# Optimization experiments

Hardware: AMD Instinct MI355X
Metric: run time of the kernel (lower is better)

Reference implementation:

```python
import jax, jax.numpy as jnp
import numpy as np

N_NODES = 100000
N_EDGES = 1600000
NUM_FEATURES = 128
NHID = 64
HIDDEN = 2 * NHID  # GATConv out_channels = nhid*2 = 128
NUM_CLASSES = 2
NUM_GRAPHS = 64
NEG_SLOPE = 0.2  # PyG GATConv default


def setup_inputs() -> dict:
    key = jax.random.key(0)
    ks = jax.random.split(key, 16)
    x = jax.random.normal(ks[0], (N_NODES, NUM_FEATURES), dtype=jnp.float32)
    edge_index = jax.random.randint(ks[1], (2, N_EDGES), 0, N_NODES, dtype=jnp.int64)
    batch = jnp.sort(jax.random.randint(ks[2], (N_NODES,), 0, NUM_GRAPHS, dtype=jnp.int64))
    def glorot(k, shape):
        lim = np.sqrt(6.0 / (shape[0] + shape[1]))
        return jax.random.uniform(k, shape, jnp.float32, -lim, lim)
    W1 = glorot(ks[3], (NUM_FEATURES, HIDDEN))
    a_src1 = glorot(ks[4], (HIDDEN, 1))[:, 0]
    a_dst1 = glorot(ks[5], (HIDDEN, 1))[:, 0]
    b1 = jnp.zeros((HIDDEN,), jnp.float32)
    W2 = glorot(ks[6], (HIDDEN, HIDDEN))
    a_src2 = glorot(ks[7], (HIDDEN, 1))[:, 0]
    a_dst2 = glorot(ks[8], (HIDDEN, 1))[:, 0]
    b2 = jnp.zeros((HIDDEN,), jnp.float32)
    fc1_w = glorot(ks[9], (HIDDEN, NHID))
    fc1_b = jnp.zeros((NHID,), jnp.float32)
    fc2_w = glorot(ks[10], (NHID, NUM_CLASSES))
    fc2_b = jnp.zeros((NUM_CLASSES,), jnp.float32)
    return {"x": x, "edge_index": edge_index, "batch": batch,
            "W1": W1, "a_src1": a_src1, "a_dst1": a_dst1, "b1": b1,
            "W2": W2, "a_src2": a_src2, "a_dst2": a_dst2, "b2": b2,
            "fc1_w": fc1_w, "fc1_b": fc1_b, "fc2_w": fc2_w, "fc2_b": fc2_b}


def gat_conv(x, src, dst, W, a_src, a_dst, b, n_nodes):
    # PyG GATConv, heads=1, add_self_loops=True: message flows src -> dst
    h = x @ W                                   # [N, H]
    alpha_s = h @ a_src                         # [N]
    alpha_d = h @ a_dst                         # [N]
    e = jax.nn.leaky_relu(alpha_s[src] + alpha_d[dst], NEG_SLOPE)  # [E2]
    m = jax.ops.segment_max(e, dst, num_segments=n_nodes)          # per-dst max
    ex = jnp.exp(e - m[dst])
    z = jax.ops.segment_sum(ex, dst, num_segments=n_nodes)
    alpha = ex / z[dst]                         # segment softmax over incoming edges
    out = jax.ops.segment_sum(h[src] * alpha[:, None], dst, num_segments=n_nodes)
    return out + b


def reference(x, edge_index, batch, W1, a_src1, a_dst1, b1,
              W2, a_src2, a_dst2, b2, fc1_w, fc1_b, fc2_w, fc2_b):
    n = x.shape[0]
    loop = jnp.arange(n, dtype=edge_index.dtype)
    src = jnp.concatenate([edge_index[0], loop])  # add self-loops (PyG default)
    dst = jnp.concatenate([edge_index[1], loop])
    h = jax.nn.selu(gat_conv(x, src, dst, W1, a_src1, a_dst1, b1, n))
    h = jax.nn.selu(gat_conv(h, src, dst, W2, a_src2, a_dst2, b2, n))
    # global mean pool over graphs
    sums = jax.ops.segment_sum(h, batch, num_segments=NUM_GRAPHS)
    cnt = jax.ops.segment_sum(jnp.ones((n,), h.dtype), batch, num_segments=NUM_GRAPHS)
    pooled = jax.nn.selu(sums / jnp.maximum(cnt, 1.0)[:, None])
    feat = jax.nn.selu(pooled @ fc1_w + fc1_b)   # dropout is identity in eval
    logits = feat @ fc2_w + fc2_b
    return logits, feat
```

## Files before the change

kernel.cpp:

```cpp
#include <hip/hip_runtime.h>
#include <hip/hip_bf16.h>

#define N_NODES 100000
#define N_EDGES 1600000
#define E_TOT   (N_EDGES + N_NODES)
#define F 128
#define NGRAPH 64
#define NEG_SLOPE 0.2f
#define SELU_SCALE 1.0507009873554805f
#define SELU_ALPHA 1.6732632423543772f

#define BSZ 256
#define NB  391
#define CAP 5120
#define CHUNK 4096
#define NCHUNK 416
#define LCAP 5120
#define PCHUNK 32

typedef __attribute__((ext_vector_type(8))) short bf16x8;
typedef __attribute__((ext_vector_type(4))) float f32x4;

__device__ __forceinline__ float selu_f(float x) {
    return x > 0.f ? SELU_SCALE * x : SELU_SCALE * SELU_ALPHA * (__expf(x) - 1.f);
}
__device__ __forceinline__ float lrelu(float x) {
    return x > 0.f ? x : NEG_SLOPE * x;
}
__device__ __forceinline__ unsigned short f2bf(float f) {
    unsigned u = __float_as_uint(f);
    return (unsigned short)((u + 0x7FFFu + ((u >> 16) & 1u)) >> 16);
}
__device__ __forceinline__ float bfval(unsigned short u) {
    return __uint_as_float(((unsigned)u) << 16);
}
__device__ __forceinline__ float ub0(unsigned w) { return (float)(w & 0xffu); }
__device__ __forceinline__ float ub1(unsigned w) { return (float)((w >> 8) & 0xffu); }
__device__ __forceinline__ float ub2(unsigned w) { return (float)((w >> 16) & 0xffu); }
__device__ __forceinline__ float ub3(unsigned w) { return (float)(w >> 24); }

__global__ __launch_bounds__(256) void init_k(int* __restrict__ cursor,
                                              float* __restrict__ gsum) {
    int i = blockIdx.x * 256 + threadIdx.x;
    if (i < NB) cursor[i] = i * CAP;
    if (i < NGRAPH * F) gsum[i] = 0.f;
}

__global__ __launch_bounds__(256) void pack_w2(const float* __restrict__ W1,
                                               const float* __restrict__ W2,
                                               unsigned short* __restrict__ W1f,
                                               unsigned short* __restrict__ W2f) {
    int i = blockIdx.x * 256 + threadIdx.x;
    const float* W = (i < 2048) ? W1 : W2;
    unsigned short* Wf = (i < 2048) ? W1f : W2f;
    int ii = i & 2047;
    int l = ii & 63, t = (ii >> 6) & 3, nt = ii >> 8;
    int kb = t * 32 + (l >> 4) * 8;
    int n  = nt * 16 + (l & 15);
    unsigned short o[8];
#pragma unroll
    for (int j = 0; j < 8; ++j) o[j] = f2bf(W[(size_t)(kb + j) * F + n]);
    uint4 p;
    p.x = ((unsigned)o[1] << 16) | o[0];
    p.y = ((unsigned)o[3] << 16) | o[2];
    p.z = ((unsigned)o[5] << 16) | o[4];
    p.w = ((unsigned)o[7] << 16) | o[6];
    ((uint4*)Wf)[ii] = p;
}

template <bool XF32>
__global__ __launch_bounds__(256) void gemm_mfma(const void* __restrict__ Xin,
                                                 const unsigned short* __restrict__ Wf,
                                                 const float* __restrict__ avs,
                                                 const float* __restrict__ avd,
                                                 unsigned char* __restrict__ Hq,
                                                 float2* __restrict__ asc,
                                                 float* __restrict__ ad_) {
    int w = threadIdx.x >> 6, l = threadIdx.x & 63;
    int row0 = blockIdx.x * 64 + w * 16;
    int arow = row0 + (l & 15);
    int arow_c = arow < N_NODES ? arow : N_NODES - 1;
    f32x4 acc[8] = {};
#pragma unroll
    for (int t = 0; t < 4; ++t) {
        bf16x8 a;
        if (XF32) {
            const float* Xf = (const float*)Xin + (size_t)arow_c * F + t * 32 + (l >> 4) * 8;
            float4 v0 = *(const float4*)Xf;
            float4 v1 = *(const float4*)(Xf + 4);
            a[0] = (short)f2bf(v0.x); a[1] = (short)f2bf(v0.y);
            a[2] = (short)f2bf(v0.z); a[3] = (short)f2bf(v0.w);
            a[4] = (short)f2bf(v1.x); a[5] = (short)f2bf(v1.y);
            a[6] = (short)f2bf(v1.z); a[7] = (short)f2bf(v1.w);
        } else {
            a = *(const bf16x8*)((const unsigned short*)Xin +
                                 (size_t)arow_c * F + t * 32 + (l >> 4) * 8);
        }
#pragma unroll
        for (int nt = 0; nt < 8; ++nt) {
            bf16x8 b = *(const bf16x8*)(Wf + (size_t)((nt * 4 + t) * 64 + l) * 8);
            acc[nt] = __builtin_amdgcn_mfma_f32_16x16x32_bf16(a, b, acc[nt], 0, 0, 0);
        }
    }
    int c = l & 15;
    float ps[4] = {}, pd[4] = {}, mx[4] = {};
#pragma unroll
    for (int nt = 0; nt < 8; ++nt) {
        float ws = avs[nt * 16 + c];
        float wd = avd[nt * 16 + c];
#pragma unroll
        for (int r = 0; r < 4; ++r) {
            ps[r] += acc[nt][r] * ws;
            pd[r] += acc[nt][r] * wd;
            mx[r] = fmaxf(mx[r], fabsf(acc[nt][r]));
        }
    }
#pragma unroll
    for (int r = 0; r < 4; ++r) {
#pragma unroll
        for (int off = 1; off < 16; off <<= 1) {
            ps[r] += __shfl_xor(ps[r], off);
            pd[r] += __shfl_xor(pd[r], off);
            mx[r] = fmaxf(mx[r], __shfl_xor(mx[r], off));
        }
    }
#pragma unroll
    for (int r = 0; r < 4; ++r) {
        int grow = row0 + (l >> 4) * 4 + r;
        if (grow >= N_NODES) continue;
        float inv = mx[r] > 0.f ? 127.f / mx[r] : 0.f;
#pragma unroll
        for (int nt = 0; nt < 8; ++nt) {
            int q = (int)rintf(acc[nt][r] * inv) + 128;
            Hq[(size_t)grow * F + nt * 16 + c] = (unsigned char)q;
        }
        if (c == 0) {
            asc[grow] = make_float2(ps[r], mx[r] * (1.f / 127.f));
            ad_[grow] = pd[r];
        }
    }
}

__global__ __launch_bounds__(256) void scatter1(const int* __restrict__ ei,
                                                int* __restrict__ cursor,
                                                unsigned* __restrict__ packed) {
    __shared__ int lh[NB], lbase[NB];
    for (int i = threadIdx.x; i < NB; i += 256) lh[i] = 0;
    __syncthreads();
    int base = blockIdx.x * CHUNK;
#pragma unroll
    for (int k = 0; k < 16; ++k) {
        int i = base + k * 256 + threadIdx.x;
        if (i < E_TOT) {
            int d = (i < N_EDGES) ? ei[N_EDGES + i] : i - N_EDGES;
            atomicAdd(&lh[d >> 8], 1);
        }
    }
    __syncthreads();
    for (int i = threadIdx.x; i < NB; i += 256) {
        int cn = lh[i];
        lbase[i] = cn ? atomicAdd(&cursor[i], cn) : 0;
        lh[i] = 0;
    }
    __syncthreads();
#pragma unroll
    for (int k = 0; k < 16; ++k) {
        int i = base + k * 256 + threadIdx.x;
        if (i < E_TOT) {
            int s, d;
            if (i < N_EDGES) { s = ei[i]; d = ei[N_EDGES + i]; }
            else             { s = d = i - N_EDGES; }
            int b = d >> 8;
            int r = atomicAdd(&lh[b], 1);
            int pos = lbase[b] + r;
            if (pos < (b + 1) * CAP)
                packed[pos] = (unsigned)s | ((unsigned)(d & 255) << 20);
        }
    }
}

__global__ __launch_bounds__(256) void build2(const int* __restrict__ cursor,
                                              const unsigned* __restrict__ packed,
                                              int2* __restrict__ rsd,
                                              int* __restrict__ csr_src) {
    __shared__ int sh_hist[BSZ], sh_row[BSZ], ts[BSZ];
    __shared__ int lsrc[LCAP];
    int b = blockIdx.x, t = threadIdx.x;
    int node0 = b << 8;
    int nn = min(BSZ, N_NODES - node0);
    int base = b * CAP;
    int cnt = min(cursor[b] - base, CAP);
    sh_hist[t] = 0;
    __syncthreads();
    for (int j = t; j < cnt; j += 256)
        atomicAdd(&sh_hist[packed[base + j] >> 20], 1);
    __syncthreads();
    int dv = sh_hist[t];
    ts[t] = dv;
    __syncthreads();
    for (int off = 1; off < 256; off <<= 1) {
        int u = (t >= off) ? ts[t - off] : 0;
        __syncthreads();
        ts[t] += u;
        __syncthreads();
    }
    sh_row[t] = ts[t] - dv;
    if (t < nn) rsd[node0 + t] = make_int2(base + sh_row[t], dv);
    sh_hist[t] = 0;
    __syncthreads();
    for (int j = t; j < cnt; j += 256) {
        unsigned u = packed[base + j];
        int dlo = u >> 20;
        int r = atomicAdd(&sh_hist[dlo], 1);
        lsrc[sh_row[dlo] + r] = (int)(u & 0xFFFFFu);
    }
    __syncthreads();
    for (int j = t; j < cnt; j += 256) csr_src[base + j] = lsrc[j];
}

__global__ __launch_bounds__(256) void gat2(const int2* __restrict__ rsd,
                                            const int* __restrict__ csr_src,
                                            const float2* __restrict__ asc,
                                            const float* __restrict__ ad_,
                                            const unsigned char* __restrict__ Hq,
                                            const float* __restrict__ bias,
                                            unsigned short* __restrict__ outb) {
    int wid = (blockIdx.x * 256 + threadIdx.x) >> 6;
    int lane = threadIdx.x & 63;
    int vbase = wid * 2;
    if (vbase >= N_NODES) return;
    const int hb = lane & 32;
    const int j  = lane & 31;
    const unsigned* HqI = (const unsigned*)Hq;
    int vown = vbase + (lane >> 5);

    int2 rv = rsd[vown];
    int start = rv.x, deg = rv.y;
    int dmax = max(deg, __shfl_xor(deg, 32));

    if (dmax <= 32) {
        int s_reg = 0;
        float2 a2 = make_float2(0.f, 0.f);
        float ev = -__builtin_inff();
        if (j < deg) {
            s_reg = csr_src[start + j];
            a2 = asc[s_reg];
            ev = lrelu(a2.x + ad_[vown]);
        }
        float m = ev;
#pragma unroll
        for (int off = 1; off < 32; off <<= 1) m = fmaxf(m, __shfl_xor(m, off));
        float ex = (j < deg) ? __expf(ev - m) : 0.f;
        float zs = ex;
#pragma unroll
        for (int off = 1; off < 32; off <<= 1) zs += __shfl_xor(zs, off);
        float alsc = (ex / zs) * a2.y;

        float acc0 = 0.f, acc1 = 0.f, acc2 = 0.f, acc3 = 0.f, ksum = 0.f;
        int e = 0;
        for (; e + 8 <= dmax; e += 8) {
            float al[8]; int sv[8]; unsigned uw[8];
#pragma unroll
            for (int q = 0; q < 8; ++q) {
                al[q] = __shfl(alsc, hb | (e + q));
                sv[q] = __shfl(s_reg, hb | (e + q));
            }
#pragma unroll
            for (int q = 0; q < 8; ++q) uw[q] = HqI[(sv[q] << 5) + j];
#pragma unroll
            for (int q = 0; q < 8; ++q) {
                ksum += al[q];
                acc0 += ub0(uw[q]) * al[q];
                acc1 += ub1(uw[q]) * al[q];
                acc2 += ub2(uw[q]) * al[q];
                acc3 += ub3(uw[q]) * al[q];
            }
        }
        for (; e < dmax; ++e) {
            float al = __shfl(alsc, hb | e);
            int   s  = __shfl(s_reg, hb | e);
            unsigned uw = HqI[(s << 5) + j];
            ksum += al;
            acc0 += ub0(uw) * al; acc1 += ub1(uw) * al;
            acc2 += ub2(uw) * al; acc3 += ub3(uw) * al;
        }
        float4 bv = *(const float4*)(bias + j * 4);
        float r0 = selu_f(acc0 - 128.f * ksum + bv.x);
        float r1 = selu_f(acc1 - 128.f * ksum + bv.y);
        float r2 = selu_f(acc2 - 128.f * ksum + bv.z);
        float r3 = selu_f(acc3 - 128.f * ksum + bv.w);
        uint2 p;
        p.x = ((unsigned)f2bf(r1) << 16) | f2bf(r0);
        p.y = ((unsigned)f2bf(r3) << 16) | f2bf(r2);
        *(uint2*)(outb + (size_t)vown * F + j * 4) = p;
    } else {
        const int half = lane >> 5;
        const int fq = lane & 31;
        for (int sub = 0; sub < 2; ++sub) {
            int vv = vbase + sub;
            int2 r2v = rsd[vv];
            int st = r2v.x, dg = r2v.y;
            float adv = ad_[vv];
            float m = -__builtin_inff();
            for (int i = st + lane; i < st + dg; i += 64)
                m = fmaxf(m, lrelu(asc[csr_src[i]].x + adv));
#pragma unroll
            for (int off = 1; off < 64; off <<= 1) m = fmaxf(m, __shfl_xor(m, off));
            float zs = 0.f;
            for (int i = st + lane; i < st + dg; i += 64)
                zs += __expf(lrelu(asc[csr_src[i]].x + adv) - m);
#pragma unroll
            for (int off = 1; off < 64; off <<= 1) zs += __shfl_xor(zs, off);
            float zinv = 1.f / zs;
            float acc0 = 0.f, acc1 = 0.f, acc2 = 0.f, acc3 = 0.f, ksum = 0.f;
            int e = 0;
            for (; e + 2 <= dg; e += 2) {
                int s = csr_src[st + e + half];
                float2 a2 = asc[s];
                float al = __expf(lrelu(a2.x + adv) - m) * zinv * a2.y;
                unsigned uw = HqI[(s << 5) + fq];
                ksum += al;
                acc0 += ub0(uw) * al; acc1 += ub1(uw) * al;
                acc2 += ub2(uw) * al; acc3 += ub3(uw) * al;
            }
            if (e < dg && half == 0) {
                int s = csr_src[st + e];
                float2 a2 = asc[s];
                float al = __expf(lrelu(a2.x + adv) - m) * zinv * a2.y;
                unsigned uw = HqI[(s << 5) + fq];
                ksum += al;
                acc0 += ub0(uw) * al; acc1 += ub1(uw) * al;
                acc2 += ub2(uw) * al; acc3 += ub3(uw) * al;
            }
            acc0 += __shfl_xor(acc0, 32); acc1 += __shfl_xor(acc1, 32);
            acc2 += __shfl_xor(acc2, 32); acc3 += __shfl_xor(acc3, 32);
            ksum += __shfl_xor(ksum, 32);
            float4 bv = *(const float4*)(bias + fq * 4);
            float r0 = selu_f(acc0 - 128.f * ksum + bv.x);
            float r1 = selu_f(acc1 - 128.f * ksum + bv.y);
            float r2 = selu_f(acc2 - 128.f * ksum + bv.z);
            float r3 = selu_f(acc3 - 128.f * ksum + bv.w);
            if (half == 0) {
                uint2 p;
                p.x = ((unsigned)f2bf(r1) << 16) | f2bf(r0);
                p.y = ((unsigned)f2bf(r3) << 16) | f2bf(r2);
                *(uint2*)(outb + (size_t)vv * F + fq * 4) = p;
            }
        }
    }
}

__device__ __forceinline__ int lower_bound(const int* __restrict__ b, int v) {
    int lo = 0, hi = N_NODES;
    while (lo < hi) { int mid = (lo + hi) >> 1; if (b[mid] < v) lo = mid + 1; else hi = mid; }
    return lo;
}

__global__ __launch_bounds__(128) void pool_partial(const unsigned short* __restrict__ Xb,
                                                    const int* __restrict__ batch,
                                                    float* __restrict__ gsum) {
    int g = blockIdx.x / PCHUNK, c = blockIdx.x % PCHUNK;
    int start = lower_bound(batch, g);
    int end = lower_bound(batch, g + 1);
    int len = end - start;
    int s0 = start + (int)((long)len * c / PCHUNK);
    int s1 = start + (int)((long)len * (c + 1) / PCHUNK);
    if (s1 <= s0) return;
    int f = threadIdx.x;
    float sum = 0.f;
    for (int i = s0; i < s1; ++i)
        sum += bfval(Xb[(size_t)i * F + f]);
    atomicAdd(&gsum[g * F + f], sum);
}

__global__ __launch_bounds__(128) void pool_head(const float* __restrict__ gsum,
                                                 const int* __restrict__ batch,
                                                 const float* __restrict__ fc1w,
                                                 const float* __restrict__ fc1b,
                                                 const float* __restrict__ fc2w,
                                                 const float* __restrict__ fc2b,
                                                 float* __restrict__ out) {
    __shared__ float pooled[128];
    __shared__ float fs[64];
    __shared__ int bnd[2];
    int g = blockIdx.x, t = threadIdx.x;
    if (t < 2) bnd[t] = lower_bound(batch, g + t);
    __syncthreads();
    float c = fmaxf((float)(bnd[1] - bnd[0]), 1.f);
    pooled[t] = selu_f(gsum[g * F + t] / c);
    __syncthreads();
    if (t < 64) {
        float a = fc1b[t];
        for (int k = 0; k < F; ++k) a += pooled[k] * fc1w[k * 64 + t];
        float fv = selu_f(a);
        fs[t] = fv;
        out[128 + g * 64 + t] = fv;
    }
    __syncthreads();
    if (t < 2) {
        float l = fc2b[t];
        for (int k = 0; k < 64; ++k) l += fs[k] * fc2w[k * 2 + t];
        out[g * 2 + t] = l;
    }
}

extern "C" void kernel_launch(void* const* d_in, const int* in_sizes, int n_in,
                              void* d_out, int out_size, void* d_ws, size_t ws_size,
                              hipStream_t stream) {
    const float* x    = (const float*)d_in[0];
    const int*   ei   = (const int*)d_in[1];
    const int*   batch= (const int*)d_in[2];
    const float* W1   = (const float*)d_in[3];
    const float* as1  = (const float*)d_in[4];
    const float* ad1  = (const float*)d_in[5];
    const float* b1   = (const float*)d_in[6];
    const float* W2   = (const float*)d_in[7];
    const float* as2  = (const float*)d_in[8];
    const float* ad2  = (const float*)d_in[9];
    const float* b2   = (const float*)d_in[10];
    const float* fc1w = (const float*)d_in[11];
    const float* fc1b = (const float*)d_in[12];
    const float* fc2w = (const float*)d_in[13];
    const float* fc2b = (const float*)d_in[14];
    float* out = (float*)d_out;

    unsigned short* Xb   = (unsigned short*)d_ws;
    unsigned char*  Hq   = (unsigned char*)(Xb + (size_t)N_NODES * F);
    unsigned short* W1f  = (unsigned short*)(Hq + (size_t)N_NODES * F);
    unsigned short* W2f  = W1f + 16384;
    float2* asc   = (float2*)(W2f + 16384);
    float*  ad_   = (float*)(asc + N_NODES);
    int2*   rsd   = (int2*)(ad_ + N_NODES);
    int*    csr_src = (int*)(rsd + N_NODES);
    unsigned* packed = (unsigned*)(csr_src + NB * CAP);
    int*    cursor= (int*)(packed + NB * CAP);
    float*  gsum  = (float*)(cursor + NB + 64);

    const int gGemm = (N_NODES + 63) / 64;
    const int gGat  = (N_NODES + 7) / 8;

    init_k<<<32, 256, 0, stream>>>(cursor, gsum);
    pack_w2<<<16, 256, 0, stream>>>(W1, W2, W1f, W2f);

    scatter1<<<NCHUNK, 256, 0, stream>>>(ei, cursor, packed);
    build2<<<NB, 256, 0, stream>>>(cursor, packed, rsd, csr_src);

    gemm_mfma<true><<<gGemm, 256, 0, stream>>>(x, W1f, as1, ad1, Hq, asc, ad_);
    gat2<<<gGat, 256, 0, stream>>>(rsd, csr_src, asc, ad_, Hq, b1, Xb);

    gemm_mfma<false><<<gGemm, 256, 0, stream>>>(Xb, W2f, as2, ad2, Hq, asc, ad_);
    gat2<<<gGat, 256, 0, stream>>>(rsd, csr_src, asc, ad_, Hq, b2, Xb);

    pool_partial<<<NGRAPH * PCHUNK, 128, 0, stream>>>(Xb, batch, gsum);
    pool_head<<<NGRAPH, 128, 0, stream>>>(gsum, batch, fc1w, fc1b, fc2w, fc2b, out);
}
```

Baseline: 217.8 us.

## Split GAT aggregation into alpha pass and feature-slabbed gather over sliced Hq

The quantized feature matrix Hq is stored as 8 column slabs of 16 bytes per node instead of 128 contiguous bytes per node. The fused gat2 kernel is split in two. alpha2 computes the per-edge softmax weights and their per-node sum and writes them with the source index into an edge array. gat_slab then gathers one slab per block, so the random-access working set per block is about 1.6 MB of Hq rather than 12.8 MB and is meant to stay cache-resident. In exchange it adds a kernel launch, writes and reads an extra edge array of roughly 13.6 MB per layer, and rereads rsd and edata once per slab.

```diff
diff --git a/kernel.cpp b/kernel.cpp
--- a/kernel.cpp
+++ b/kernel.cpp
@@ -17,6 +17,7 @@
 #define NCHUNK 416
 #define LCAP 5120
 #define PCHUNK 32
+#define NSLAB 8
 
 typedef __attribute__((ext_vector_type(8))) short bf16x8;
 typedef __attribute__((ext_vector_type(4))) float f32x4;
@@ -132,7 +133,7 @@
 #pragma unroll
         for (int nt = 0; nt < 8; ++nt) {
             int q = (int)rintf(acc[nt][r] * inv) + 128;
-            Hq[(size_t)grow * F + nt * 16 + c] = (unsigned char)q;
+            Hq[(size_t)nt * N_NODES * 16 + (size_t)grow * 16 + c] = (unsigned char)q;
         }
         if (c == 0) {
             asc[grow] = make_float2(ps[r], mx[r] * (1.f / 127.f));
@@ -218,20 +219,17 @@
     for (int j = t; j < cnt; j += 256) csr_src[base + j] = lsrc[j];
 }
 
-__global__ __launch_bounds__(256) void gat2(const int2* __restrict__ rsd,
-                                            const int* __restrict__ csr_src,
-                                            const float2* __restrict__ asc,
-                                            const float* __restrict__ ad_,
-                                            const unsigned char* __restrict__ Hq,
-                                            const float* __restrict__ bias,
-                                            unsigned short* __restrict__ outb) {
+__global__ __launch_bounds__(256) void alpha2(const int2* __restrict__ rsd,
+                                              const int* __restrict__ csr_src,
+                                              const float2* __restrict__ asc,
+                                              const float* __restrict__ ad_,
+                                              uint2* __restrict__ edata,
+                                              float* __restrict__ ksum_) {
     int wid = (blockIdx.x * 256 + threadIdx.x) >> 6;
     int lane = threadIdx.x & 63;
     int vbase = wid * 2;
     if (vbase >= N_NODES) return;
-    const int hb = lane & 32;
-    const int j  = lane & 31;
-    const unsigned* HqI = (const unsigned*)Hq;
+    int j = lane & 31;
     int vown = vbase + (lane >> 5);
 
     int2 rv = rsd[vown];
@@ -255,47 +253,12 @@
 #pragma unroll
         for (int off = 1; off < 32; off <<= 1) zs += __shfl_xor(zs, off);
         float alsc = (ex / zs) * a2.y;
-
-        float acc0 = 0.f, acc1 = 0.f, acc2 = 0.f, acc3 = 0.f, ksum = 0.f;
-        int e = 0;
-        for (; e + 8 <= dmax; e += 8) {
-            float al[8]; int sv[8]; unsigned uw[8];
-#pragma unroll
-            for (int q = 0; q < 8; ++q) {
-                al[q] = __shfl(alsc, hb | (e + q));
-                sv[q] = __shfl(s_reg, hb | (e + q));
-            }
-#pragma unroll
-            for (int q = 0; q < 8; ++q) uw[q] = HqI[(sv[q] << 5) + j];
-#pragma unroll
-            for (int q = 0; q < 8; ++q) {
-                ksum += al[q];
-                acc0 += ub0(uw[q]) * al[q];
-                acc1 += ub1(uw[q]) * al[q];
-                acc2 += ub2(uw[q]) * al[q];
-                acc3 += ub3(uw[q]) * al[q];
-            }
-        }
-        for (; e < dmax; ++e) {
-            float al = __shfl(alsc, hb | e);
-            int   s  = __shfl(s_reg, hb | e);
-            unsigned uw = HqI[(s << 5) + j];
-            ksum += al;
-            acc0 += ub0(uw) * al; acc1 += ub1(uw) * al;
-            acc2 += ub2(uw) * al; acc3 += ub3(uw) * al;
-        }
-        float4 bv = *(const float4*)(bias + j * 4);
-        float r0 = selu_f(acc0 - 128.f * ksum + bv.x);
-        float r1 = selu_f(acc1 - 128.f * ksum + bv.y);
-        float r2 = selu_f(acc2 - 128.f * ksum + bv.z);
-        float r3 = selu_f(acc3 - 128.f * ksum + bv.w);
-        uint2 p;
-        p.x = ((unsigned)f2bf(r1) << 16) | f2bf(r0);
-        p.y = ((unsigned)f2bf(r3) << 16) | f2bf(r2);
-        *(uint2*)(outb + (size_t)vown * F + j * 4) = p;
+        float ks = alsc;
+#pragma unroll
+        for (int off = 1; off < 32; off <<= 1) ks += __shfl_xor(ks, off);
+        if (j < deg) edata[start + j] = make_uint2(__float_as_uint(alsc), (unsigned)s_reg);
+        if (j == 0) ksum_[vown] = ks;
     } else {
-        const int half = lane >> 5;
-        const int fq = lane & 31;
         for (int sub = 0; sub < 2; ++sub) {
             int vv = vbase + sub;
             int2 r2v = rsd[vv];
@@ -312,40 +275,62 @@
 #pragma unroll
             for (int off = 1; off < 64; off <<= 1) zs += __shfl_xor(zs, off);
             float zinv = 1.f / zs;
-            float acc0 = 0.f, acc1 = 0.f, acc2 = 0.f, acc3 = 0.f, ksum = 0.f;
-            int e = 0;
-            for (; e + 2 <= dg; e += 2) {
-                int s = csr_src[st + e + half];
+            float ksp = 0.f;
+            for (int i = st + lane; i < st + dg; i += 64) {
+                int s = csr_src[i];
                 float2 a2 = asc[s];
                 float al = __expf(lrelu(a2.x + adv) - m) * zinv * a2.y;
-                unsigned uw = HqI[(s << 5) + fq];
-                ksum += al;
-                acc0 += ub0(uw) * al; acc1 += ub1(uw) * al;
-                acc2 += ub2(uw) * al; acc3 += ub3(uw) * al;
+                edata[i] = make_uint2(__float_as_uint(al), (unsigned)s);
+                ksp += al;
             }
-            if (e < dg && half == 0) {
-                int s = csr_src[st + e];
-                float2 a2 = asc[s];
-                float al = __expf(lrelu(a2.x + adv) - m) * zinv * a2.y;
-                unsigned uw = HqI[(s << 5) + fq];
-                ksum += al;
-                acc0 += ub0(uw) * al; acc1 += ub1(uw) * al;
-                acc2 += ub2(uw) * al; acc3 += ub3(uw) * al;
-            }
-            acc0 += __shfl_xor(acc0, 32); acc1 += __shfl_xor(acc1, 32);
-            acc2 += __shfl_xor(acc2, 32); acc3 += __shfl_xor(acc3, 32);
-            ksum += __shfl_xor(ksum, 32);
-            float4 bv = *(const float4*)(bias + fq * 4);
-            float r0 = selu_f(acc0 - 128.f * ksum + bv.x);
-            float r1 = selu_f(acc1 - 128.f * ksum + bv.y);
-            float r2 = selu_f(acc2 - 128.f * ksum + bv.z);
-            float r3 = selu_f(acc3 - 128.f * ksum + bv.w);
-            if (half == 0) {
-                uint2 p;
-                p.x = ((unsigned)f2bf(r1) << 16) | f2bf(r0);
-                p.y = ((unsigned)f2bf(r3) << 16) | f2bf(r2);
-                *(uint2*)(outb + (size_t)vv * F + fq * 4) = p;
-            }
+#pragma unroll
+            for (int off = 1; off < 64; off <<= 1) ksp += __shfl_xor(ksp, off);
+            if (lane == 0) ksum_[vv] = ksp;
+        }
+    }
+}
+
+__global__ __launch_bounds__(256) void gat_slab(const int2* __restrict__ rsd,
+                                                const uint2* __restrict__ edata,
+                                                const float* __restrict__ ksum_,
+                                                const unsigned char* __restrict__ Hq,
+                                                const float* __restrict__ bias,
+                                                unsigned short* __restrict__ outb) {
+    int slab = blockIdx.x & 7;
+    int nb = blockIdx.x >> 3;
+    int w = threadIdx.x >> 6, l = threadIdx.x & 63;
+    int e16 = l >> 2, d = l & 3;
+    const unsigned* HqI = (const unsigned*)(Hq + (size_t)slab * N_NODES * 16);
+    float4 bv = *(const float4*)(bias + slab * 16 + d * 4);
+
+    for (int i = 0; i < 16; ++i) {
+        int v = nb * 64 + w * 16 + i;
+        if (v >= N_NODES) break;
+        int2 rv = rsd[v];
+        int start = rv.x, deg = rv.y;
+        float a0 = 0.f, a1 = 0.f, a2 = 0.f, a3 = 0.f;
+        for (int e = e16; e < deg; e += 16) {
+            uint2 ed = edata[start + e];
+            float al = __uint_as_float(ed.x);
+            unsigned uw = HqI[(int)ed.y * 4 + d];
+            a0 += ub0(uw) * al; a1 += ub1(uw) * al;
+            a2 += ub2(uw) * al; a3 += ub3(uw) * al;
+        }
+#pragma unroll
+        for (int off = 4; off < 64; off <<= 1) {
+            a0 += __shfl_xor(a0, off); a1 += __shfl_xor(a1, off);
+            a2 += __shfl_xor(a2, off); a3 += __shfl_xor(a3, off);
+        }
+        if (e16 == 0) {
+            float K = 128.f * ksum_[v];
+            float r0 = selu_f(a0 - K + bv.x);
+            float r1 = selu_f(a1 - K + bv.y);
+            float r2 = selu_f(a2 - K + bv.z);
+            float r3 = selu_f(a3 - K + bv.w);
+            uint2 p;
+            p.x = ((unsigned)f2bf(r1) << 16) | f2bf(r0);
+            p.y = ((unsigned)f2bf(r3) << 16) | f2bf(r2);
+            *(uint2*)(outb + (size_t)v * F + slab * 16 + d * 4) = p;
         }
     }
 }
@@ -430,14 +415,17 @@
     unsigned short* W2f  = W1f + 16384;
     float2* asc   = (float2*)(W2f + 16384);
     float*  ad_   = (float*)(asc + N_NODES);
-    int2*   rsd   = (int2*)(ad_ + N_NODES);
+    float*  ksum_ = ad_ + N_NODES;
+    int2*   rsd   = (int2*)(ksum_ + N_NODES);
     int*    csr_src = (int*)(rsd + N_NODES);
     unsigned* packed = (unsigned*)(csr_src + NB * CAP);
-    int*    cursor= (int*)(packed + NB * CAP);
+    uint2*  edata = (uint2*)(packed + (size_t)NB * CAP);
+    int*    cursor= (int*)(edata + E_TOT);
     float*  gsum  = (float*)(cursor + NB + 64);
 
     const int gGemm = (N_NODES + 63) / 64;
-    const int gGat  = (N_NODES + 7) / 8;
+    const int gAl   = (N_NODES + 7) / 8;
+    const int gSlab = gGemm * NSLAB;
 
     init_k<<<32, 256, 0, stream>>>(cursor, gsum);
     pack_w2<<<16, 256, 0, stream>>>(W1, W2, W1f, W2f);
@@ -446,10 +434,12 @@
     build2<<<NB, 256, 0, stream>>>(cursor, packed, rsd, csr_src);
 
     gemm_mfma<true><<<gGemm, 256, 0, stream>>>(x, W1f, as1, ad1, Hq, asc, ad_);
-    gat2<<<gGat, 256, 0, stream>>>(rsd, csr_src, asc, ad_, Hq, b1, Xb);
+    alpha2<<<gAl, 256, 0, stream>>>(rsd, csr_src, asc, ad_, edata, ksum_);
+    gat_slab<<<gSlab, 256, 0, stream>>>(rsd, edata, ksum_, Hq, b1, Xb);
 
     gemm_mfma<false><<<gGemm, 256, 0, stream>>>(Xb, W2f, as2, ad2, Hq, asc, ad_);
-    gat2<<<gGat, 256, 0, stream>>>(rsd, csr_src, asc, ad_, Hq, b2, Xb);
+    alpha2<<<gAl, 256, 0, stream>>>(rsd, csr_src, asc, ad_, edata, ksum_);
+    gat_slab<<<gSlab, 256, 0, stream>>>(rsd, edata, ksum_, Hq, b2, Xb);
 
     pool_partial<<<NGRAPH * PCHUNK, 128, 0, stream>>>(Xb, batch, gsum);
     pool_head<<<NGRAPH, 128, 0, stream>>>(gsum, batch, fc1w, fc1b, fc2w, fc2b, out);
```

Result: slower. 546.0 us (+150.7%).
